# Kernel tuning notes

Hardware: AMD Instinct MI355X
Metric: run time of the kernel (lower is better)

## Reference

```python
import jax, jax.numpy as jnp
import numpy as np

N_NODES = 100000
N_EDGES = 1600000
IN_C, HID_C, OUT_C = 128, 128, 64


def gcn_conv(x, src, dst, W, b, num_nodes):
    # PyG GCNConv: add self-loops, symmetric normalization, linear transform,
    # aggregate source features into targets.
    h = x @ W  # [N, C_out]
    loop = jnp.arange(num_nodes, dtype=src.dtype)
    s = jnp.concatenate([src, loop])
    d = jnp.concatenate([dst, loop])
    deg = jax.ops.segment_sum(jnp.ones_like(d, dtype=h.dtype), d, num_segments=num_nodes)
    inv_sqrt = jnp.where(deg > 0, jax.lax.rsqrt(deg), 0.0)
    norm = inv_sqrt[s] * inv_sqrt[d]  # [E+N]
    msgs = h[s] * norm[:, None]  # gather + scale
    out = jax.ops.segment_sum(msgs, d, num_segments=num_nodes)  # scatter-add
    return out + b


def setup_inputs() -> dict:
    key = jax.random.key(0)
    k1, k2, k3, k4 = jax.random.split(key, 4)
    x = jax.random.normal(k1, (N_NODES, IN_C), dtype=jnp.float32)
    edge_index = jax.random.randint(k2, (2, N_EDGES), 0, N_NODES, dtype=jnp.int64)
    W1 = jax.random.normal(k3, (IN_C, HID_C), dtype=jnp.float32) * (1.0 / np.sqrt(IN_C))
    b1 = jnp.zeros((HID_C,), dtype=jnp.float32)
    W2 = jax.random.normal(k4, (HID_C, OUT_C), dtype=jnp.float32) * (1.0 / np.sqrt(HID_C))
    b2 = jnp.zeros((OUT_C,), dtype=jnp.float32)
    return {"x": x, "edge_index": edge_index, "W1": W1, "b1": b1, "W2": W2, "b2": b2}


def reference(x, edge_index, W1, b1, W2, b2):
    num_nodes = x.shape[0]
    src, dst = edge_index[0], edge_index[1]  # PyG flow: source -> target
    h = gcn_conv(x, src, dst, W1, b1, num_nodes)
    h = jax.nn.relu(h)  # dropout is identity in eval mode
    out = gcn_conv(h, src, dst, W2, b2, num_nodes)
    return out
```

## Files before the change

### kernel.cpp

```cpp
#include <hip/hip_runtime.h>

#define IN_C 128
#define HID_C 128
#define OUT_C 64

#define BSPAN 256
#define BCAP  5120
#define NBMAX 512
#define ACHUNK 4096

typedef unsigned int uint32;
typedef unsigned short ushort16;
typedef _Float16 f16;
typedef f16   f16x8 __attribute__((ext_vector_type(8)));
typedef float f32x4 __attribute__((ext_vector_type(4)));


__device__ __forceinline__ ushort16 f2bf(float f) {
    union { float f; uint32 u; } v; v.f = f;
    uint32 r = v.u + 0x7FFFu + ((v.u >> 16) & 1u);
    return (ushort16)(r >> 16);
}

__device__ __forceinline__ void unpack2(uint32 u, float& f0, float& f1) {
    union { uint32 x; float f; } a, b;
    a.x = u << 16;
    b.x = u & 0xFFFF0000u;
    f0 = a.f; f1 = b.f;
}

__device__ __forceinline__ void acc_row(uint4 r, float* acc) {
    float f0, f1;
    unpack2(r.x, f0, f1); acc[0] += f0; acc[1] += f1;
    unpack2(r.y, f0, f1); acc[2] += f0; acc[3] += f1;
    unpack2(r.z, f0, f1); acc[4] += f0; acc[5] += f1;
    unpack2(r.w, f0, f1); acc[6] += f0; acc[7] += f1;
}


__launch_bounds__(256)
__global__ void bin_edges_kernel(const int* __restrict__ src, const int* __restrict__ dst,
                                 int* __restrict__ bucketCur, uint32* __restrict__ binned,
                                 int E, int nbuck) {
    __shared__ int hist[NBMAX];
    __shared__ int base[NBMAX];
    const int tid = threadIdx.x;
    const int e0  = blockIdx.x * ACHUNK;

    for (int i = tid; i < NBMAX; i += 256) hist[i] = 0;
    __syncthreads();

    int d[16], s[16], rk[16];
#pragma unroll
    for (int j = 0; j < 16; j++) {
        int e = e0 + j * 256 + tid;
        if (e < E) {
            d[j] = dst[e];
            s[j] = src[e];
            rk[j] = atomicAdd(&hist[d[j] >> 8], 1);
        } else d[j] = -1;
    }
    __syncthreads();

    for (int b = tid; b < nbuck; b += 256) {
        int h = hist[b];
        base[b] = h ? atomicAdd(&bucketCur[b], h) : 0;
    }
    __syncthreads();

#pragma unroll
    for (int j = 0; j < 16; j++) {
        if (d[j] >= 0) {
            int b = d[j] >> 8;
            int pos = base[b] + rk[j];
            if (pos < BCAP)
                binned[(size_t)b * BCAP + pos] =
                    ((uint32)(d[j] & 255) << 17) | (uint32)s[j];
        }
    }
}


__launch_bounds__(256)
__global__ void bucket_csr_kernel(const uint32* __restrict__ binned,
                                  const int* __restrict__ bucketCur,
                                  int* __restrict__ csr_src, int* __restrict__ rowbeg,
                                  int* __restrict__ rowend, float* __restrict__ inv, int N) {
    constexpr int MAXIT = BCAP / 256;
    __shared__ int cnt[BSPAN];
    __shared__ int scn[BSPAN];
    __shared__ int excl[BSPAN];
    const int b   = blockIdx.x;
    const int tid = threadIdx.x;
    const int n0  = b * BSPAN;
    const int ne  = min(bucketCur[b], BCAP);
    const uint32* bp = binned + (size_t)b * BCAP;

    cnt[tid] = 0;
    __syncthreads();

    uint32 ebuf[MAXIT];
    int    rbuf[MAXIT];
    int nmine = 0;
    for (int i = tid; i < ne; i += 256) {
        uint32 e = bp[i];
        ebuf[nmine] = e;
        rbuf[nmine] = atomicAdd(&cnt[e >> 17], 1);
        nmine++;
    }
    __syncthreads();

    int v = cnt[tid];
    scn[tid] = v;
    __syncthreads();
    for (int off = 1; off < 256; off <<= 1) {
        int u = (tid >= off) ? scn[tid - off] : 0;
        __syncthreads();
        scn[tid] += u;
        __syncthreads();
    }
    int ex = scn[tid] - v;
    excl[tid] = ex;

    int n = n0 + tid;
    if (n < N) {
        int gb = b * BCAP + ex;
        rowbeg[n] = gb;
        rowend[n] = gb + v;
        inv[n] = rsqrtf((float)(v + 1));
    }
    __syncthreads();

    for (int j = 0; j < nmine; j++) {
        uint32 e = ebuf[j];
        csr_src[(size_t)b * BCAP + excl[e >> 17] + rbuf[j]] = (int)(e & 0x1FFFFu);
    }
}


template <int C>
__device__ __forceinline__ void wprep_one(const float* __restrict__ W, f16* __restrict__ Wf, int t) {
    constexpr int NCT = C / 16;
    int lane = t & 63;
    int ctkc = t >> 6;
    int ct = ctkc % NCT, kc = ctkc / NCT;
    int kbase = kc * 32 + (lane >> 4) * 8;
    int col   = ct * 16 + (lane & 15);
    f16 v[8];
#pragma unroll
    for (int j = 0; j < 8; j++) v[j] = (f16)W[(size_t)(kbase + j) * C + col];
    *(uint4*)(Wf + (size_t)t * 8) = *(const uint4*)v;
}

__global__ void wprep_both(const float* __restrict__ W1, f16* __restrict__ Wf1,
                           const float* __restrict__ W2, f16* __restrict__ Wf2,
                           int* __restrict__ bucketCur, int nbuck) {
    constexpr int T1 = 4 * (HID_C / 16) * 64;
    constexpr int T2 = 4 * (OUT_C / 16) * 64;
    int t = blockIdx.x * 256 + threadIdx.x;
    if (t < nbuck) bucketCur[t] = 0;
    if (t < T1)            wprep_one<HID_C>(W1, Wf1, t);
    else if (t < T1 + T2)  wprep_one<OUT_C>(W2, Wf2, t - T1);
}


template <int C>
__launch_bounds__(256)
__global__ void mfma_gemm(const float* __restrict__ X, const f16* __restrict__ Wf,
                          const float* __restrict__ inv, ushort16* __restrict__ outb, int N) {
    constexpr int NCT = C / 16;
    __shared__ __align__(16) f16 As[4 * 4 * 64 * 8];
    __shared__ __align__(16) f16 Bs[4 * NCT * 64 * 8];

    const int tid  = threadIdx.x;
    const int lane = tid & 63;
    const int w    = tid >> 6;
    const int row0 = blockIdx.x * 64;

    {
        constexpr int TOT = 4 * NCT * 64 * 8;
        const uint4* src = (const uint4*)Wf;
        uint4* dst = (uint4*)Bs;
#pragma unroll
        for (int i = 0; i < TOT / 8 / 256; i++)
            dst[tid + i * 256] = src[tid + i * 256];
    }

    {
        int r   = tid >> 2;
        int seg = tid & 3;
        int row = row0 + r;
        int ws_ = r >> 4;
        int r15 = r & 15;
#pragma unroll
        for (int i = 0; i < 8; i++) {
            int k = seg * 32 + i * 4;
            float4 v = make_float4(0.f, 0.f, 0.f, 0.f);
            if (row < N) v = *(const float4*)(X + (size_t)row * 128 + k);
            int q = (k >> 3) & 3, j0 = k & 7;
            f16 h[4] = {(f16)v.x, (f16)v.y, (f16)v.z, (f16)v.w};
            int slot = ((seg * 4 + ws_) * 64 + (q * 16 + r15)) * 8 + j0;
            *(uint2*)(As + slot) = *(const uint2*)h;
        }
    }
    __syncthreads();

    f32x4 acc[NCT];
#pragma unroll
    for (int c = 0; c < NCT; c++) acc[c] = (f32x4){0.f, 0.f, 0.f, 0.f};
#pragma unroll
    for (int kc = 0; kc < 4; kc++) {
        f16x8 a = *(const f16x8*)&As[((kc * 4 + w) * 64 + lane) * 8];
#pragma unroll
        for (int ct = 0; ct < NCT; ct++) {
            f16x8 b = *(const f16x8*)&Bs[((kc * NCT + ct) * 64 + lane) * 8];
            acc[ct] = __builtin_amdgcn_mfma_f32_16x16x32_f16(a, b, acc[ct], 0, 0, 0);
        }
    }

    __syncthreads();
    ushort16* Ds = (ushort16*)As;
    const int q = lane >> 4;
    float iv[4];
#pragma unroll
    for (int reg = 0; reg < 4; reg++) {
        int row = row0 + w * 16 + q * 4 + reg;
        iv[reg] = (row < N) ? inv[row] : 0.f;
    }
#pragma unroll
    for (int ct = 0; ct < NCT; ct++) {
#pragma unroll
        for (int reg = 0; reg < 4; reg++) {
            int r = w * 16 + q * 4 + reg;
            Ds[r * C + ct * 16 + (lane & 15)] = f2bf(acc[ct][reg] * iv[reg]);
        }
    }
    __syncthreads();
    {
        int r  = tid >> 2;
        int row = row0 + r;
        if (row < N) {
            constexpr int SPT = C / 4;
            int c0 = (tid & 3) * SPT;
            const uint4* s = (const uint4*)&Ds[r * C + c0];
            uint4* d = (uint4*)(outb + (size_t)row * C + c0);
#pragma unroll
            for (int i = 0; i < SPT / 8; i++) d[i] = s[i];
        }
    }
}


__launch_bounds__(256)
__global__ void fused_gather_gemm(const int* __restrict__ rowbeg, const int* __restrict__ rowend,
                                  const int* __restrict__ csr,
                                  const ushort16* __restrict__ hsb,
                                  const float* __restrict__ inv, const float* __restrict__ bias1,
                                  const f16* __restrict__ Wf2,
                                  ushort16* __restrict__ outb, int N) {
    constexpr int CIN = 128, COUT = 64, NCT = COUT / 16;
    __shared__ __align__(16) f16 As[4 * 4 * 64 * 8];
    __shared__ __align__(16) f16 Bs[4 * NCT * 64 * 8];

    const int tid  = threadIdx.x;
    const int lane = tid & 63;
    const int w    = tid >> 6;
    const int row0 = blockIdx.x * 64;

    {
        constexpr int TOT = 4 * NCT * 64 * 8;
        const uint4* s = (const uint4*)Wf2;
        uint4* d = (uint4*)Bs;
#pragma unroll
        for (int i = 0; i < TOT / 8 / 256; i++)
            d[tid + i * 256] = s[tid + i * 256];
    }

    {
        int r = tid >> 2;
        int q = tid & 3;
        int n = row0 + r;
        float acc[32];
#pragma unroll
        for (int j = 0; j < 32; j++) acc[j] = 0.f;

        if (n < N) {
            const ushort16* base = hsb + (size_t)n * CIN + q * 32;
            uint4 s0 = *(const uint4*)(base);
            uint4 s1 = *(const uint4*)(base + 8);
            uint4 s2 = *(const uint4*)(base + 16);
            uint4 s3 = *(const uint4*)(base + 24);
            acc_row(s0, acc); acc_row(s1, acc + 8); acc_row(s2, acc + 16); acc_row(s3, acc + 24);

            int beg = rowbeg[n], end = rowend[n];
            int i = beg;
            for (; i + 2 <= end; i += 2) {
                const ushort16* p0 = hsb + (size_t)csr[i]     * CIN + q * 32;
                const ushort16* p1 = hsb + (size_t)csr[i + 1] * CIN + q * 32;
                uint4 a0 = *(const uint4*)(p0);
                uint4 a1 = *(const uint4*)(p0 + 8);
                uint4 a2 = *(const uint4*)(p0 + 16);
                uint4 a3 = *(const uint4*)(p0 + 24);
                uint4 b0 = *(const uint4*)(p1);
                uint4 b1 = *(const uint4*)(p1 + 8);
                uint4 b2 = *(const uint4*)(p1 + 16);
                uint4 b3 = *(const uint4*)(p1 + 24);
                acc_row(a0, acc); acc_row(a1, acc + 8); acc_row(a2, acc + 16); acc_row(a3, acc + 24);
                acc_row(b0, acc); acc_row(b1, acc + 8); acc_row(b2, acc + 16); acc_row(b3, acc + 24);
            }
            if (i < end) {
                const ushort16* p0 = hsb + (size_t)csr[i] * CIN + q * 32;
                uint4 a0 = *(const uint4*)(p0);
                uint4 a1 = *(const uint4*)(p0 + 8);
                uint4 a2 = *(const uint4*)(p0 + 16);
                uint4 a3 = *(const uint4*)(p0 + 24);
                acc_row(a0, acc); acc_row(a1, acc + 8); acc_row(a2, acc + 16); acc_row(a3, acc + 24);
            }

            float iv = inv[n];
#pragma unroll
            for (int j = 0; j < 32; j++)
                acc[j] = fmaxf(fmaf(iv, acc[j], bias1[q * 32 + j]), 0.f);
        }

        int ws_ = r >> 4, r15 = r & 15;
#pragma unroll
        for (int i8 = 0; i8 < 4; i8++) {
            f16 h[8];
#pragma unroll
            for (int j = 0; j < 8; j++) h[j] = (f16)acc[i8 * 8 + j];
            int slot = ((q * 4 + ws_) * 64 + (i8 * 16 + r15)) * 8;
            *(uint4*)(As + slot) = *(const uint4*)h;
        }
    }
    __syncthreads();

    f32x4 acc2[NCT];
#pragma unroll
    for (int c = 0; c < NCT; c++) acc2[c] = (f32x4){0.f, 0.f, 0.f, 0.f};
#pragma unroll
    for (int kc = 0; kc < 4; kc++) {
        f16x8 a = *(const f16x8*)&As[((kc * 4 + w) * 64 + lane) * 8];
#pragma unroll
        for (int ct = 0; ct < NCT; ct++) {
            f16x8 b = *(const f16x8*)&Bs[((kc * NCT + ct) * 64 + lane) * 8];
            acc2[ct] = __builtin_amdgcn_mfma_f32_16x16x32_f16(a, b, acc2[ct], 0, 0, 0);
        }
    }

    __syncthreads();
    ushort16* Ds = (ushort16*)As;
    const int q2 = lane >> 4;
    float iv2[4];
#pragma unroll
    for (int reg = 0; reg < 4; reg++) {
        int row = row0 + w * 16 + q2 * 4 + reg;
        iv2[reg] = (row < N) ? inv[row] : 0.f;
    }
#pragma unroll
    for (int ct = 0; ct < NCT; ct++) {
#pragma unroll
        for (int reg = 0; reg < 4; reg++) {
            int r = w * 16 + q2 * 4 + reg;
            Ds[r * COUT + ct * 16 + (lane & 15)] = f2bf(acc2[ct][reg] * iv2[reg]);
        }
    }
    __syncthreads();
    {
        int r   = tid >> 2;
        int row = row0 + r;
        if (row < N) {
            constexpr int SPT = COUT / 4;
            int c0 = (tid & 3) * SPT;
            const uint4* s = (const uint4*)&Ds[r * COUT + c0];
            uint4* d = (uint4*)(outb + (size_t)row * COUT + c0);
#pragma unroll
            for (int i = 0; i < SPT / 8; i++) d[i] = s[i];
        }
    }
}


template <int C, bool RELU>
__launch_bounds__(256)
__global__ void gather_agg_bf16(const int* __restrict__ rowbeg, const int* __restrict__ rowend,
                                const int* __restrict__ csr_src,
                                const ushort16* __restrict__ hsb, const float* __restrict__ inv,
                                const float* __restrict__ b, float* __restrict__ out, int N) {
    constexpr int TPN = C / 8;
    constexpr int NPB = 256 / TPN;
    int n    = blockIdx.x * NPB + threadIdx.x / TPN;
    int lane = threadIdx.x % TPN;
    if (n >= N) return;
    int c8 = lane * 8;

    float acc[8];
    {
        uint4 raw = *(const uint4*)(hsb + (size_t)n * C + c8);
        unpack2(raw.x, acc[0], acc[1]);
        unpack2(raw.y, acc[2], acc[3]);
        unpack2(raw.z, acc[4], acc[5]);
        unpack2(raw.w, acc[6], acc[7]);
    }

    int beg = rowbeg[n];
    int end = rowend[n];
    int i = beg;
    for (; i + 4 <= end; i += 4) {
        int s0 = csr_src[i];
        int s1 = csr_src[i + 1];
        int s2 = csr_src[i + 2];
        int s3 = csr_src[i + 3];
        uint4 r0 = *(const uint4*)(hsb + (size_t)s0 * C + c8);
        uint4 r1 = *(const uint4*)(hsb + (size_t)s1 * C + c8);
        uint4 r2 = *(const uint4*)(hsb + (size_t)s2 * C + c8);
        uint4 r3 = *(const uint4*)(hsb + (size_t)s3 * C + c8);
        acc_row(r0, acc); acc_row(r1, acc); acc_row(r2, acc); acc_row(r3, acc);
    }
    for (; i < end; i++) {
        uint4 r0 = *(const uint4*)(hsb + (size_t)csr_src[i] * C + c8);
        acc_row(r0, acc);
    }

    float iv = inv[n];
    float4 b0 = *(const float4*)(b + c8);
    float4 b1 = *(const float4*)(b + c8 + 4);
    float r[8];
    r[0] = fmaf(iv, acc[0], b0.x); r[1] = fmaf(iv, acc[1], b0.y);
    r[2] = fmaf(iv, acc[2], b0.z); r[3] = fmaf(iv, acc[3], b0.w);
    r[4] = fmaf(iv, acc[4], b1.x); r[5] = fmaf(iv, acc[5], b1.y);
    r[6] = fmaf(iv, acc[6], b1.z); r[7] = fmaf(iv, acc[7], b1.w);
    if (RELU) {
#pragma unroll
        for (int j = 0; j < 8; j++) r[j] = fmaxf(r[j], 0.f);
    }
    float* po = out + (size_t)n * C + c8;
    *(float4*)(po)     = make_float4(r[0], r[1], r[2], r[3]);
    *(float4*)(po + 4) = make_float4(r[4], r[5], r[6], r[7]);
}

extern "C" void kernel_launch(void* const* d_in, const int* in_sizes, int n_in,
                              void* d_out, int out_size, void* d_ws, size_t ws_size,
                              hipStream_t stream) {
    const float* x  = (const float*)d_in[0];
    const int*   ei = (const int*)d_in[1];
    const float* W1 = (const float*)d_in[2];
    const float* b1 = (const float*)d_in[3];
    const float* W2 = (const float*)d_in[4];
    const float* b2 = (const float*)d_in[5];
    float* out = (float*)d_out;

    const int N = in_sizes[0] / IN_C;
    const int E = in_sizes[1] / 2;
    const int* src = ei;
    const int* dst = ei + E;
    const int nbuck = (N + BSPAN - 1) / BSPAN;

    char* ws = (char*)d_ws;
    auto align_up = [](size_t v) { return (v + 1023) & ~(size_t)1023; };
    size_t off = 0;
    int*      bucketCur = (int*)(ws + off);      off += align_up((size_t)nbuck * sizeof(int));
    float*    inv       = (float*)(ws + off);    off += align_up((size_t)N * sizeof(float));
    int*      rowbeg    = (int*)(ws + off);      off += align_up((size_t)N * sizeof(int));
    int*      rowend    = (int*)(ws + off);      off += align_up((size_t)N * sizeof(int));
    uint32*   binned    = (uint32*)(ws + off);   off += align_up((size_t)nbuck * BCAP * sizeof(uint32));
    int*      csrs      = (int*)(ws + off);      off += align_up((size_t)nbuck * BCAP * sizeof(int));
    f16*      Wf1       = (f16*)(ws + off);      off += align_up((size_t)4 * (HID_C/16) * 64 * 8 * sizeof(f16));
    f16*      Wf2       = (f16*)(ws + off);      off += align_up((size_t)4 * (OUT_C/16) * 64 * 8 * sizeof(f16));
    ushort16* hs1b      = (ushort16*)(ws + off); off += align_up((size_t)N * HID_C * sizeof(ushort16));
    ushort16* hs2b      = (ushort16*)(ws + off); off += align_up((size_t)N * OUT_C * sizeof(ushort16));

    wprep_both<<<(4 * (HID_C/16 + OUT_C/16) * 64 + 255) / 256, 256, 0, stream>>>(
        W1, Wf1, W2, Wf2, bucketCur, nbuck);
    bin_edges_kernel<<<(E + ACHUNK - 1) / ACHUNK, 256, 0, stream>>>(
        src, dst, bucketCur, binned, E, nbuck);
    bucket_csr_kernel<<<nbuck, 256, 0, stream>>>(
        binned, bucketCur, csrs, rowbeg, rowend, inv, N);

    mfma_gemm<HID_C><<<(N + 63) / 64, 256, 0, stream>>>(x, Wf1, inv, hs1b, N);

    fused_gather_gemm<<<(N + 63) / 64, 256, 0, stream>>>(
        rowbeg, rowend, csrs, hs1b, inv, b1, Wf2, hs2b, N);

    {
        constexpr int NPB = 256 / (OUT_C / 8);
        gather_agg_bf16<OUT_C, false><<<(N + NPB - 1) / NPB, 256, 0, stream>>>(
            rowbeg, rowend, csrs, hs2b, inv, b2, out, N);
    }
}
```

Before: 261.1 us.

## Merge preprocessing and GEMM1 kernels, move source-side normalization into gather

Weight prep now runs inside the edge-binning kernel as extra blocks, and bucket CSR construction runs in the same grid as the first GEMM. The GEMM no longer depends on inv, so it can run in parallel with CSR building. To allow that, the first GEMM stops pre-scaling rows by inv, and the fused gather scales each neighbor row by inv[src] through an extra indexed load per edge. Weight fragments are read straight from global memory instead of being staged in LDS, and the bucket counter reset moves to hipMemsetAsync. This removes launches and serialization at the cost of more per-edge work and a memset call.

```diff
diff --git a/kernel.cpp b/kernel.cpp
--- a/kernel.cpp
+++ b/kernel.cpp
@@ -37,106 +37,13 @@
     unpack2(r.w, f0, f1); acc[6] += f0; acc[7] += f1;
 }
 
-
-__launch_bounds__(256)
-__global__ void bin_edges_kernel(const int* __restrict__ src, const int* __restrict__ dst,
-                                 int* __restrict__ bucketCur, uint32* __restrict__ binned,
-                                 int E, int nbuck) {
-    __shared__ int hist[NBMAX];
-    __shared__ int base[NBMAX];
-    const int tid = threadIdx.x;
-    const int e0  = blockIdx.x * ACHUNK;
-
-    for (int i = tid; i < NBMAX; i += 256) hist[i] = 0;
-    __syncthreads();
-
-    int d[16], s[16], rk[16];
-#pragma unroll
-    for (int j = 0; j < 16; j++) {
-        int e = e0 + j * 256 + tid;
-        if (e < E) {
-            d[j] = dst[e];
-            s[j] = src[e];
-            rk[j] = atomicAdd(&hist[d[j] >> 8], 1);
-        } else d[j] = -1;
-    }
-    __syncthreads();
-
-    for (int b = tid; b < nbuck; b += 256) {
-        int h = hist[b];
-        base[b] = h ? atomicAdd(&bucketCur[b], h) : 0;
-    }
-    __syncthreads();
-
-#pragma unroll
-    for (int j = 0; j < 16; j++) {
-        if (d[j] >= 0) {
-            int b = d[j] >> 8;
-            int pos = base[b] + rk[j];
-            if (pos < BCAP)
-                binned[(size_t)b * BCAP + pos] =
-                    ((uint32)(d[j] & 255) << 17) | (uint32)s[j];
-        }
-    }
-}
-
-
-__launch_bounds__(256)
-__global__ void bucket_csr_kernel(const uint32* __restrict__ binned,
-                                  const int* __restrict__ bucketCur,
-                                  int* __restrict__ csr_src, int* __restrict__ rowbeg,
-                                  int* __restrict__ rowend, float* __restrict__ inv, int N) {
-    constexpr int MAXIT = BCAP / 256;
-    __shared__ int cnt[BSPAN];
-    __shared__ int scn[BSPAN];
-    __shared__ int excl[BSPAN];
-    const int b   = blockIdx.x;
-    const int tid = threadIdx.x;
-    const int n0  = b * BSPAN;
-    const int ne  = min(bucketCur[b], BCAP);
-    const uint32* bp = binned + (size_t)b * BCAP;
-
-    cnt[tid] = 0;
-    __syncthreads();
-
-    uint32 ebuf[MAXIT];
-    int    rbuf[MAXIT];
-    int nmine = 0;
-    for (int i = tid; i < ne; i += 256) {
-        uint32 e = bp[i];
-        ebuf[nmine] = e;
-        rbuf[nmine] = atomicAdd(&cnt[e >> 17], 1);
-        nmine++;
-    }
-    __syncthreads();
-
-    int v = cnt[tid];
-    scn[tid] = v;
-    __syncthreads();
-    for (int off = 1; off < 256; off <<= 1) {
-        int u = (tid >= off) ? scn[tid - off] : 0;
-        __syncthreads();
-        scn[tid] += u;
-        __syncthreads();
-    }
-    int ex = scn[tid] - v;
-    excl[tid] = ex;
-
-    int n = n0 + tid;
-    if (n < N) {
-        int gb = b * BCAP + ex;
-        rowbeg[n] = gb;
-        rowend[n] = gb + v;
-        inv[n] = rsqrtf((float)(v + 1));
-    }
-    __syncthreads();
-
-    for (int j = 0; j < nmine; j++) {
-        uint32 e = ebuf[j];
-        csr_src[(size_t)b * BCAP + excl[e >> 17] + rbuf[j]] = (int)(e & 0x1FFFFu);
-    }
-}
-
+__device__ __forceinline__ void acc_row_s(uint4 r, float s, float* acc) {
+    float f0, f1;
+    unpack2(r.x, f0, f1); acc[0] = fmaf(s, f0, acc[0]); acc[1] = fmaf(s, f1, acc[1]);
+    unpack2(r.y, f0, f1); acc[2] = fmaf(s, f0, acc[2]); acc[3] = fmaf(s, f1, acc[3]);
+    unpack2(r.z, f0, f1); acc[4] = fmaf(s, f0, acc[4]); acc[5] = fmaf(s, f1, acc[5]);
+    unpack2(r.w, f0, f1); acc[6] = fmaf(s, f0, acc[6]); acc[7] = fmaf(s, f1, acc[7]);
+}
 
 template <int C>
 __device__ __forceinline__ void wprep_one(const float* __restrict__ W, f16* __restrict__ Wf, int t) {
@@ -152,39 +59,118 @@
     *(uint4*)(Wf + (size_t)t * 8) = *(const uint4*)v;
 }
 
-__global__ void wprep_both(const float* __restrict__ W1, f16* __restrict__ Wf1,
-                           const float* __restrict__ W2, f16* __restrict__ Wf2,
-                           int* __restrict__ bucketCur, int nbuck) {
-    constexpr int T1 = 4 * (HID_C / 16) * 64;
-    constexpr int T2 = 4 * (OUT_C / 16) * 64;
-    int t = blockIdx.x * 256 + threadIdx.x;
-    if (t < nbuck) bucketCur[t] = 0;
-    if (t < T1)            wprep_one<HID_C>(W1, Wf1, t);
-    else if (t < T1 + T2)  wprep_one<OUT_C>(W2, Wf2, t - T1);
-}
-
-
-template <int C>
+
 __launch_bounds__(256)
-__global__ void mfma_gemm(const float* __restrict__ X, const f16* __restrict__ Wf,
-                          const float* __restrict__ inv, ushort16* __restrict__ outb, int N) {
-    constexpr int NCT = C / 16;
+__global__ void k1_bin_wprep(const int* __restrict__ src, const int* __restrict__ dst,
+                             int* __restrict__ bucketCur, uint32* __restrict__ binned,
+                             const float* __restrict__ W1, f16* __restrict__ Wf1,
+                             const float* __restrict__ W2, f16* __restrict__ Wf2,
+                             int E, int nbuck, int nchunk) {
+    const int tid = threadIdx.x;
+    if ((int)blockIdx.x >= nchunk) {
+        int t = ((int)blockIdx.x - nchunk) * 256 + tid;
+        constexpr int T1 = 4 * (HID_C / 16) * 64;
+        constexpr int T2 = 4 * (OUT_C / 16) * 64;
+        if (t < T1)           wprep_one<HID_C>(W1, Wf1, t);
+        else if (t < T1 + T2) wprep_one<OUT_C>(W2, Wf2, t - T1);
+        return;
+    }
+    __shared__ int hist[NBMAX];
+    __shared__ int base[NBMAX];
+    const int e0 = blockIdx.x * ACHUNK;
+
+    for (int i = tid; i < NBMAX; i += 256) hist[i] = 0;
+    __syncthreads();
+
+    int d[16], s[16], rk[16];
+#pragma unroll
+    for (int j = 0; j < 16; j++) {
+        int e = e0 + j * 256 + tid;
+        if (e < E) {
+            d[j] = dst[e];
+            s[j] = src[e];
+            rk[j] = atomicAdd(&hist[d[j] >> 8], 1);
+        } else d[j] = -1;
+    }
+    __syncthreads();
+
+    for (int b = tid; b < nbuck; b += 256) {
+        int h = hist[b];
+        base[b] = h ? atomicAdd(&bucketCur[b], h) : 0;
+    }
+    __syncthreads();
+
+#pragma unroll
+    for (int j = 0; j < 16; j++) {
+        if (d[j] >= 0) {
+            int b = d[j] >> 8;
+            int pos = base[b] + rk[j];
+            if (pos < BCAP)
+                binned[(size_t)b * BCAP + pos] =
+                    ((uint32)(d[j] & 255) << 17) | (uint32)s[j];
+        }
+    }
+}
+
+
+__launch_bounds__(256)
+__global__ void k2_csr_gemm1(const uint32* __restrict__ binned, const int* __restrict__ bucketCur,
+                             int* __restrict__ csrs, int* __restrict__ rowbeg,
+                             int* __restrict__ rowend, float* __restrict__ inv,
+                             const float* __restrict__ x, const f16* __restrict__ Wf1,
+                             ushort16* __restrict__ hs1b, int N, int nbuck) {
     __shared__ __align__(16) f16 As[4 * 4 * 64 * 8];
-    __shared__ __align__(16) f16 Bs[4 * NCT * 64 * 8];
-
-    const int tid  = threadIdx.x;
+    const int tid = threadIdx.x;
+
+    if ((int)blockIdx.x < nbuck) {
+        int* cnt = (int*)As;
+        int* scn = cnt + BSPAN;
+        int* ex  = scn + BSPAN;
+        const int b  = blockIdx.x;
+        const int ne = min(bucketCur[b], BCAP);
+        const uint32* bp = binned + (size_t)b * BCAP;
+
+        cnt[tid] = 0;
+        __syncthreads();
+
+        int rbuf[BCAP / 256];
+        int nm = 0;
+        for (int i = tid; i < ne; i += 256)
+            rbuf[nm++] = atomicAdd(&cnt[bp[i] >> 17], 1);
+        __syncthreads();
+
+        int v = cnt[tid];
+        scn[tid] = v;
+        __syncthreads();
+        for (int off = 1; off < 256; off <<= 1) {
+            int u = (tid >= off) ? scn[tid - off] : 0;
+            __syncthreads();
+            scn[tid] += u;
+            __syncthreads();
+        }
+        int e0 = scn[tid] - v;
+        ex[tid] = e0;
+
+        int n = b * BSPAN + tid;
+        if (n < N) {
+            int gb = b * BCAP + e0;
+            rowbeg[n] = gb;
+            rowend[n] = gb + v;
+            inv[n] = rsqrtf((float)(v + 1));
+        }
+        __syncthreads();
+
+        nm = 0;
+        for (int i = tid; i < ne; i += 256) {
+            uint32 e = bp[i];
+            csrs[(size_t)b * BCAP + ex[e >> 17] + rbuf[nm++]] = (int)(e & 0x1FFFFu);
+        }
+        return;
+    }
+
     const int lane = tid & 63;
     const int w    = tid >> 6;
-    const int row0 = blockIdx.x * 64;
-
-    {
-        constexpr int TOT = 4 * NCT * 64 * 8;
-        const uint4* src = (const uint4*)Wf;
-        uint4* dst = (uint4*)Bs;
-#pragma unroll
-        for (int i = 0; i < TOT / 8 / 256; i++)
-            dst[tid + i * 256] = src[tid + i * 256];
-    }
+    const int row0 = ((int)blockIdx.x - nbuck) * 64;
 
     {
         int r   = tid >> 2;
@@ -196,7 +182,7 @@
         for (int i = 0; i < 8; i++) {
             int k = seg * 32 + i * 4;
             float4 v = make_float4(0.f, 0.f, 0.f, 0.f);
-            if (row < N) v = *(const float4*)(X + (size_t)row * 128 + k);
+            if (row < N) v = *(const float4*)(x + (size_t)row * 128 + k);
             int q = (k >> 3) & 3, j0 = k & 7;
             f16 h[4] = {(f16)v.x, (f16)v.y, (f16)v.z, (f16)v.w};
             int slot = ((seg * 4 + ws_) * 64 + (q * 16 + r15)) * 8 + j0;
@@ -205,15 +191,15 @@
     }
     __syncthreads();
 
-    f32x4 acc[NCT];
-#pragma unroll
-    for (int c = 0; c < NCT; c++) acc[c] = (f32x4){0.f, 0.f, 0.f, 0.f};
+    f32x4 acc[8];
+#pragma unroll
+    for (int c = 0; c < 8; c++) acc[c] = (f32x4){0.f, 0.f, 0.f, 0.f};
 #pragma unroll
     for (int kc = 0; kc < 4; kc++) {
         f16x8 a = *(const f16x8*)&As[((kc * 4 + w) * 64 + lane) * 8];
 #pragma unroll
-        for (int ct = 0; ct < NCT; ct++) {
-            f16x8 b = *(const f16x8*)&Bs[((kc * NCT + ct) * 64 + lane) * 8];
+        for (int ct = 0; ct < 8; ct++) {
+            f16x8 b = *(const f16x8*)&Wf1[(size_t)(((kc * 8 + ct) * 64) + lane) * 8];
             acc[ct] = __builtin_amdgcn_mfma_f32_16x16x32_f16(a, b, acc[ct], 0, 0, 0);
         }
     }
@@ -221,46 +207,36 @@
     __syncthreads();
     ushort16* Ds = (ushort16*)As;
     const int q = lane >> 4;
-    float iv[4];
-#pragma unroll
-    for (int reg = 0; reg < 4; reg++) {
-        int row = row0 + w * 16 + q * 4 + reg;
-        iv[reg] = (row < N) ? inv[row] : 0.f;
-    }
-#pragma unroll
-    for (int ct = 0; ct < NCT; ct++) {
+#pragma unroll
+    for (int ct = 0; ct < 8; ct++)
 #pragma unroll
         for (int reg = 0; reg < 4; reg++) {
             int r = w * 16 + q * 4 + reg;
-            Ds[r * C + ct * 16 + (lane & 15)] = f2bf(acc[ct][reg] * iv[reg]);
-        }
-    }
-    __syncthreads();
-    {
-        int r  = tid >> 2;
+            Ds[r * 128 + ct * 16 + (lane & 15)] = f2bf(acc[ct][reg]);
+        }
+    __syncthreads();
+    {
+        int r   = tid >> 2;
         int row = row0 + r;
         if (row < N) {
-            constexpr int SPT = C / 4;
-            int c0 = (tid & 3) * SPT;
-            const uint4* s = (const uint4*)&Ds[r * C + c0];
-            uint4* d = (uint4*)(outb + (size_t)row * C + c0);
-#pragma unroll
-            for (int i = 0; i < SPT / 8; i++) d[i] = s[i];
+            int c0 = (tid & 3) * 32;
+            const uint4* s = (const uint4*)&Ds[r * 128 + c0];
+            uint4* d = (uint4*)(hs1b + (size_t)row * 128 + c0);
+#pragma unroll
+            for (int i = 0; i < 4; i++) d[i] = s[i];
         }
     }
 }
 
 
 __launch_bounds__(256)
-__global__ void fused_gather_gemm(const int* __restrict__ rowbeg, const int* __restrict__ rowend,
-                                  const int* __restrict__ csr,
-                                  const ushort16* __restrict__ hsb,
-                                  const float* __restrict__ inv, const float* __restrict__ bias1,
-                                  const f16* __restrict__ Wf2,
-                                  ushort16* __restrict__ outb, int N) {
-    constexpr int CIN = 128, COUT = 64, NCT = COUT / 16;
+__global__ void k3_fused(const int* __restrict__ rowbeg, const int* __restrict__ rowend,
+                         const int* __restrict__ csrs,
+                         const ushort16* __restrict__ hs1b, const float* __restrict__ inv,
+                         const float* __restrict__ b1, const f16* __restrict__ Wf2,
+                         ushort16* __restrict__ hs2b, int N) {
+    constexpr int NCT = OUT_C / 16;
     __shared__ __align__(16) f16 As[4 * 4 * 64 * 8];
-    __shared__ __align__(16) f16 Bs[4 * NCT * 64 * 8];
 
     const int tid  = threadIdx.x;
     const int lane = tid & 63;
@@ -268,15 +244,6 @@
     const int row0 = blockIdx.x * 64;
 
     {
-        constexpr int TOT = 4 * NCT * 64 * 8;
-        const uint4* s = (const uint4*)Wf2;
-        uint4* d = (uint4*)Bs;
-#pragma unroll
-        for (int i = 0; i < TOT / 8 / 256; i++)
-            d[tid + i * 256] = s[tid + i * 256];
-    }
-
-    {
         int r = tid >> 2;
         int q = tid & 3;
         int n = row0 + r;
@@ -285,42 +252,50 @@
         for (int j = 0; j < 32; j++) acc[j] = 0.f;
 
         if (n < N) {
-            const ushort16* base = hsb + (size_t)n * CIN + q * 32;
+            float ivn = inv[n];
+            const ushort16* base = hs1b + (size_t)n * 128 + q * 32;
             uint4 s0 = *(const uint4*)(base);
             uint4 s1 = *(const uint4*)(base + 8);
             uint4 s2 = *(const uint4*)(base + 16);
             uint4 s3 = *(const uint4*)(base + 24);
-            acc_row(s0, acc); acc_row(s1, acc + 8); acc_row(s2, acc + 16); acc_row(s3, acc + 24);
+            acc_row_s(s0, ivn, acc);      acc_row_s(s1, ivn, acc + 8);
+            acc_row_s(s2, ivn, acc + 16); acc_row_s(s3, ivn, acc + 24);
 
             int beg = rowbeg[n], end = rowend[n];
             int i = beg;
             for (; i + 2 <= end; i += 2) {
-                const ushort16* p0 = hsb + (size_t)csr[i]     * CIN + q * 32;
-                const ushort16* p1 = hsb + (size_t)csr[i + 1] * CIN + q * 32;
+                int e0 = csrs[i], e1 = csrs[i + 1];
+                float v0 = inv[e0], v1 = inv[e1];
+                const ushort16* p0 = hs1b + (size_t)e0 * 128 + q * 32;
+                const ushort16* p1 = hs1b + (size_t)e1 * 128 + q * 32;
                 uint4 a0 = *(const uint4*)(p0);
                 uint4 a1 = *(const uint4*)(p0 + 8);
                 uint4 a2 = *(const uint4*)(p0 + 16);
                 uint4 a3 = *(const uint4*)(p0 + 24);
-                uint4 b0 = *(const uint4*)(p1);
-                uint4 b1 = *(const uint4*)(p1 + 8);
-                uint4 b2 = *(const uint4*)(p1 + 16);
-                uint4 b3 = *(const uint4*)(p1 + 24);
-                acc_row(a0, acc); acc_row(a1, acc + 8); acc_row(a2, acc + 16); acc_row(a3, acc + 24);
-                acc_row(b0, acc); acc_row(b1, acc + 8); acc_row(b2, acc + 16); acc_row(b3, acc + 24);
+                uint4 c0 = *(const uint4*)(p1);
+                uint4 c1 = *(const uint4*)(p1 + 8);
+                uint4 c2 = *(const uint4*)(p1 + 16);
+                uint4 c3 = *(const uint4*)(p1 + 24);
+                acc_row_s(a0, v0, acc);      acc_row_s(a1, v0, acc + 8);
+                acc_row_s(a2, v0, acc + 16); acc_row_s(a3, v0, acc + 24);
+                acc_row_s(c0, v1, acc);      acc_row_s(c1, v1, acc + 8);
+                acc_row_s(c2, v1, acc + 16); acc_row_s(c3, v1, acc + 24);
             }
             if (i < end) {
-                const ushort16* p0 = hsb + (size_t)csr[i] * CIN + q * 32;
+                int e0 = csrs[i];
+                float v0 = inv[e0];
+                const ushort16* p0 = hs1b + (size_t)e0 * 128 + q * 32;
                 uint4 a0 = *(const uint4*)(p0);
                 uint4 a1 = *(const uint4*)(p0 + 8);
                 uint4 a2 = *(const uint4*)(p0 + 16);
                 uint4 a3 = *(const uint4*)(p0 + 24);
-                acc_row(a0, acc); acc_row(a1, acc + 8); acc_row(a2, acc + 16); acc_row(a3, acc + 24);
+                acc_row_s(a0, v0, acc);      acc_row_s(a1, v0, acc + 8);
+                acc_row_s(a2, v0, acc + 16); acc_row_s(a3, v0, acc + 24);
             }
 
-            float iv = inv[n];
 #pragma unroll
             for (int j = 0; j < 32; j++)
-                acc[j] = fmaxf(fmaf(iv, acc[j], bias1[q * 32 + j]), 0.f);
+                acc[j] = fmaxf(fmaf(ivn, acc[j], b1[q * 32 + j]), 0.f);
         }
 
         int ws_ = r >> 4, r15 = r & 15;
@@ -343,7 +318,7 @@
         f16x8 a = *(const f16x8*)&As[((kc * 4 + w) * 64 + lane) * 8];
 #pragma unroll
         for (int ct = 0; ct < NCT; ct++) {
-            f16x8 b = *(const f16x8*)&Bs[((kc * NCT + ct) * 64 + lane) * 8];
+            f16x8 b = *(const f16x8*)&Wf2[(size_t)(((kc * NCT + ct) * 64) + lane) * 8];
             acc2[ct] = __builtin_amdgcn_mfma_f32_16x16x32_f16(a, b, acc2[ct], 0, 0, 0);
         }
     }
@@ -358,24 +333,22 @@
         iv2[reg] = (row < N) ? inv[row] : 0.f;
     }
 #pragma unroll
-    for (int ct = 0; ct < NCT; ct++) {
+    for (int ct = 0; ct < NCT; ct++)
 #pragma unroll
         for (int reg = 0; reg < 4; reg++) {
             int r = w * 16 + q2 * 4 + reg;
-            Ds[r * COUT + ct * 16 + (lane & 15)] = f2bf(acc2[ct][reg] * iv2[reg]);
-        }
-    }
+            Ds[r * 64 + ct * 16 + (lane & 15)] = f2bf(acc2[ct][reg] * iv2[reg]);
+        }
     __syncthreads();
     {
         int r   = tid >> 2;
         int row = row0 + r;
         if (row < N) {
-            constexpr int SPT = COUT / 4;
-            int c0 = (tid & 3) * SPT;
-            const uint4* s = (const uint4*)&Ds[r * COUT + c0];
-            uint4* d = (uint4*)(outb + (size_t)row * COUT + c0);
-#pragma unroll
-            for (int i = 0; i < SPT / 8; i++) d[i] = s[i];
+            int c0 = (tid & 3) * 16;
+            const uint4* s = (const uint4*)&Ds[r * 64 + c0];
+            uint4* d = (uint4*)(hs2b + (size_t)row * 64 + c0);
+#pragma unroll
+            for (int i = 0; i < 2; i++) d[i] = s[i];
         }
     }
 }
@@ -454,7 +427,10 @@
     const int E = in_sizes[1] / 2;
     const int* src = ei;
     const int* dst = ei + E;
-    const int nbuck = (N + BSPAN - 1) / BSPAN;
+    const int nbuck  = (N + BSPAN - 1) / BSPAN;
+    const int nchunk = (E + ACHUNK - 1) / ACHUNK;
+    const int ntile  = (N + 63) / 64;
+    const int wpb    = (4 * (HID_C/16 + OUT_C/16) * 64 + 255) / 256;
 
     char* ws = (char*)d_ws;
     auto align_up = [](size_t v) { return (v + 1023) & ~(size_t)1023; };
@@ -470,16 +446,15 @@
     ushort16* hs1b      = (ushort16*)(ws + off); off += align_up((size_t)N * HID_C * sizeof(ushort16));
     ushort16* hs2b      = (ushort16*)(ws + off); off += align_up((size_t)N * OUT_C * sizeof(ushort16));
 
-    wprep_both<<<(4 * (HID_C/16 + OUT_C/16) * 64 + 255) / 256, 256, 0, stream>>>(
-        W1, Wf1, W2, Wf2, bucketCur, nbuck);
-    bin_edges_kernel<<<(E + ACHUNK - 1) / ACHUNK, 256, 0, stream>>>(
-        src, dst, bucketCur, binned, E, nbuck);
-    bucket_csr_kernel<<<nbuck, 256, 0, stream>>>(
-        binned, bucketCur, csrs, rowbeg, rowend, inv, N);
-
-    mfma_gemm<HID_C><<<(N + 63) / 64, 256, 0, stream>>>(x, Wf1, inv, hs1b, N);
-
-    fused_gather_gemm<<<(N + 63) / 64, 256, 0, stream>>>(
+    hipMemsetAsync(bucketCur, 0, (size_t)nbuck * sizeof(int), stream);
+
+    k1_bin_wprep<<<nchunk + wpb, 256, 0, stream>>>(
+        src, dst, bucketCur, binned, W1, Wf1, W2, Wf2, E, nbuck, nchunk);
+
+    k2_csr_gemm1<<<nbuck + ntile, 256, 0, stream>>>(
+        binned, bucketCur, csrs, rowbeg, rowend, inv, x, Wf1, hs1b, N, nbuck);
+
+    k3_fused<<<ntile, 256, 0, stream>>>(
         rowbeg, rowend, csrs, hs1b, inv, b1, Wf2, hs2b, N);
 
     {
```

Result: slower. 269.6 us (+3.3%).
